# Kernel optimization log

Measured on AMD Instinct MI355X. Metric: run time of the kernel, lower is better.

## Reference

```python
import jax, jax.numpy as jnp
import numpy as np

X_DIM, Y_DIM, HIDDEN, N = 768, 768, 300, 768


def setup_inputs() -> dict:
    key = jax.random.key(0)
    ks = jax.random.split(key, 7)
    lim1 = 1.0 / np.sqrt(X_DIM + Y_DIM)
    lim2 = 1.0 / np.sqrt(HIDDEN)
    return {
        "x_samples": jax.random.normal(ks[0], (N, X_DIM), dtype=jnp.float32),
        "y_samples": jax.random.normal(ks[1], (N, Y_DIM), dtype=jnp.float32),
        "perm": jax.random.permutation(ks[2], N).astype(jnp.int32),
        # Linear 1: (x_dim+y_dim) -> hidden, torch default uniform init
        "W1": jax.random.uniform(ks[3], (HIDDEN, X_DIM + Y_DIM), jnp.float32, -lim1, lim1),
        "b1": jax.random.uniform(ks[4], (HIDDEN,), jnp.float32, -lim1, lim1),
        # Linear 2: hidden -> 1
        "W2": jax.random.uniform(ks[5], (1, HIDDEN), jnp.float32, -lim2, lim2),
        "b2": jax.random.uniform(ks[6], (1,), jnp.float32, -lim2, lim2),
    }


def reference(x_samples, y_samples, perm, W1, b1, W2, b2):
    n = x_samples.shape[0]
    x_dim = x_samples.shape[1]
    # First linear is separable across the concat: split W1 into x- and y-parts.
    hx = x_samples @ W1[:, :x_dim].T            # [N, H]
    hy = y_samples @ W1[:, x_dim:].T            # [N, H]
    w2 = W2[0]                                   # [H]
    # T0: matched pairs (x_i, y_i)
    t0 = jax.nn.softplus(jax.nn.relu(hx + hy + b1) @ w2 + b2[0])   # [N]
    # T1[i, j] = F(x_j, y_perm[i]) -- pairwise tile, [N, N, H] intermediate
    hyp = hy[perm]                               # [N, H]
    hpair = jax.nn.relu(hyp[:, None, :] + hx[None, :, :] + b1)     # [N, N, H]
    t1 = jax.nn.softplus(hpair @ w2 + b2[0])     # [N, N]
    lower_bound = t0.mean() - (jax.nn.logsumexp(t1, axis=1).mean() - jnp.log(n).astype(t1.dtype))
    return lower_bound
```

## Files before the change

kernel.cpp:

```cpp
#include <hip/hip_runtime.h>
#include <math.h>

#define NN   768
#define HH   300
#define LDH  304
#define KD   768
#define SZ   (NN*LDH)


__global__ __launch_bounds__(256) void k1_gemm(
    const float* __restrict__ x, const float* __restrict__ y,
    const int* __restrict__ perm, const float* __restrict__ W1,
    float* __restrict__ wsf)
{
    const int tid = threadIdx.x;
    const int tx = tid & 15, ty = tid >> 4;
    const int i0 = blockIdx.x * 32;
    const int h0 = blockIdx.y * 64;
    const int gemm = blockIdx.z & 1;
    const int kh   = blockIdx.z >> 1;
    const int k_beg = kh * 384;

    const float* src = gemm ? y : x;
    const int koff = gemm ? KD : 0;

    __shared__ float xs[32][34];
    __shared__ float ws[32][68];

    float acc[2][4] = {{0,0,0,0},{0,0,0,0}};

    const int srow = tid >> 3, sc4 = (tid & 7) << 2;
    int grow = i0 + srow;
    if (gemm) grow = perm[grow];
    const float* srcp = src + (size_t)grow * KD + sc4 + k_beg;

    const int hrow = tid >> 2, kc8 = (tid & 3) << 3;
    const int hg = h0 + hrow;
    const bool hvalid = hg < HH;
    const float* wrow = W1 + (size_t)hg * (2*KD) + koff + kc8 + k_beg;

    for (int kc = 0; kc < 384; kc += 32) {
        float4 xv = *(const float4*)(srcp + kc);
        xs[sc4+0][srow] = xv.x; xs[sc4+1][srow] = xv.y;
        xs[sc4+2][srow] = xv.z; xs[sc4+3][srow] = xv.w;

        float4 w0 = make_float4(0,0,0,0), w1 = make_float4(0,0,0,0);
        if (hvalid) {
            w0 = *(const float4*)(wrow + kc);
            w1 = *(const float4*)(wrow + kc + 4);
        }
        ws[kc8+0][hrow]=w0.x; ws[kc8+1][hrow]=w0.y; ws[kc8+2][hrow]=w0.z; ws[kc8+3][hrow]=w0.w;
        ws[kc8+4][hrow]=w1.x; ws[kc8+5][hrow]=w1.y; ws[kc8+6][hrow]=w1.z; ws[kc8+7][hrow]=w1.w;
        __syncthreads();

        #pragma unroll
        for (int k = 0; k < 32; ++k) {
            float a0 = xs[k][2*ty], a1 = xs[k][2*ty+1];
            float b0 = ws[k][4*tx+0], b1v = ws[k][4*tx+1];
            float b2v = ws[k][4*tx+2], b3v = ws[k][4*tx+3];
            acc[0][0] = fmaf(a0,b0, acc[0][0]); acc[0][1] = fmaf(a0,b1v,acc[0][1]);
            acc[0][2] = fmaf(a0,b2v,acc[0][2]); acc[0][3] = fmaf(a0,b3v,acc[0][3]);
            acc[1][0] = fmaf(a1,b0, acc[1][0]); acc[1][1] = fmaf(a1,b1v,acc[1][1]);
            acc[1][2] = fmaf(a1,b2v,acc[1][2]); acc[1][3] = fmaf(a1,b3v,acc[1][3]);
        }
        __syncthreads();
    }

    float* dst = wsf + (gemm ? 2*(size_t)SZ : 0) + (size_t)kh * SZ;
    #pragma unroll
    for (int r = 0; r < 2; ++r) {
        int gi = i0 + 2*ty + r;
        #pragma unroll
        for (int c = 0; c < 4; ++c) {
            int hh = h0 + 4*tx + c;
            if (hh < HH) dst[(size_t)gi*LDH + hh] = acc[r][c];
        }
    }
}

__global__ __launch_bounds__(256) void k1b_combine(
    const float* __restrict__ b1, float* __restrict__ wsf)
{
    const int N4 = SZ/4;
    int idx = blockIdx.x * 256 + threadIdx.x;
    int which = idx >= N4 ? 1 : 0;
    int rem = idx - which * N4;
    int base = rem * 4;
    int h = base % LDH;
    const float* p0 = wsf + (which ? 2*(size_t)SZ : 0);
    const float* p1 = p0 + SZ;
    float* dst = wsf + (which ? 5*(size_t)SZ : 4*(size_t)SZ);

    float4 out = make_float4(0,0,0,0);
    if (h < HH) {
        float4 v0 = *(const float4*)(p0 + base);
        float4 v1 = *(const float4*)(p1 + base);
        out.x = v0.x + v1.x; out.y = v0.y + v1.y;
        out.z = v0.z + v1.z; out.w = v0.w + v1.w;
        if (which) {
            float4 bv = *(const float4*)(b1 + h);
            out.x += bv.x; out.y += bv.y; out.z += bv.z; out.w += bv.w;
        }
    }
    *(float4*)(dst + base) = out;
}

__global__ __launch_bounds__(256) void k2_pair(
    const float* __restrict__ wsf, const float* __restrict__ w2,
    const float* __restrict__ b2, float* __restrict__ esum)
{
    const int tid = threadIdx.x;
    const int tx = tid & 15, ty = tid >> 4;
    const int i0 = blockIdx.x * 32;
    const int j0 = blockIdx.y * 64;

    const float* Af = wsf + 5*(size_t)SZ;
    const float* Cf = wsf + 4*(size_t)SZ;

    __shared__ float As[60][34];
    __shared__ float Cs[60][68];
    __shared__ float ws2[60];

    float acc[2][4] = {{0,0,0,0},{0,0,0,0}};

    for (int hc = 0; hc < HH; hc += 60) {
        for (int e = tid; e < 480; e += 256) {
            int i = e / 15, h4 = (e % 15) * 4;
            float4 v = *(const float4*)(Af + (size_t)(i0 + i)*LDH + hc + h4);
            As[h4+0][i] = v.x; As[h4+1][i] = v.y; As[h4+2][i] = v.z; As[h4+3][i] = v.w;
        }
        for (int e = tid; e < 960; e += 256) {
            int j = e / 15, h4 = (e % 15) * 4;
            float4 v = *(const float4*)(Cf + (size_t)(j0 + j)*LDH + hc + h4);
            Cs[h4+0][j] = v.x; Cs[h4+1][j] = v.y; Cs[h4+2][j] = v.z; Cs[h4+3][j] = v.w;
        }
        if (tid < 60) ws2[tid] = w2[hc + tid];
        __syncthreads();

        #pragma unroll 6
        for (int h = 0; h < 60; ++h) {
            float wh = ws2[h];
            float a0 = As[h][2*ty], a1 = As[h][2*ty+1];
            float4 cv = *(const float4*)&Cs[h][4*tx];
            float t;
            t = fmaxf(a0+cv.x,0.f); acc[0][0] = fmaf(t,wh,acc[0][0]);
            t = fmaxf(a0+cv.y,0.f); acc[0][1] = fmaf(t,wh,acc[0][1]);
            t = fmaxf(a0+cv.z,0.f); acc[0][2] = fmaf(t,wh,acc[0][2]);
            t = fmaxf(a0+cv.w,0.f); acc[0][3] = fmaf(t,wh,acc[0][3]);
            t = fmaxf(a1+cv.x,0.f); acc[1][0] = fmaf(t,wh,acc[1][0]);
            t = fmaxf(a1+cv.y,0.f); acc[1][1] = fmaf(t,wh,acc[1][1]);
            t = fmaxf(a1+cv.z,0.f); acc[1][2] = fmaf(t,wh,acc[1][2]);
            t = fmaxf(a1+cv.w,0.f); acc[1][3] = fmaf(t,wh,acc[1][3]);
        }
        __syncthreads();
    }

    const float b2v = b2[0];
    #pragma unroll
    for (int r = 0; r < 2; ++r) {
        float s = expf(acc[r][0] + b2v) + expf(acc[r][1] + b2v)
                + expf(acc[r][2] + b2v) + expf(acc[r][3] + b2v);
        s += __shfl_xor(s, 1);
        s += __shfl_xor(s, 2);
        s += __shfl_xor(s, 4);
        s += __shfl_xor(s, 8);
        if (tx == 0) atomicAdd(&esum[i0 + 2*ty + r], s);
    }
}

__global__ __launch_bounds__(256) void k2b_t0(
    const float* __restrict__ wsf, const int* __restrict__ perm,
    const float* __restrict__ w2, const float* __restrict__ b2,
    float* __restrict__ t0out)
{
    const int lane = threadIdx.x & 63;
    const int row  = blockIdx.x * 4 + (threadIdx.x >> 6);
    const float* Af = wsf + 5*(size_t)SZ;
    const float* Cf = wsf + 4*(size_t)SZ;
    const int pr = perm[row];

    float acc = 0.f;
    for (int h = lane; h < HH; h += 64) {
        float a = Af[(size_t)row*LDH + h];
        float c = Cf[(size_t)pr *LDH + h];
        float z = fmaxf(a + c, 0.f);
        acc = fmaf(z, w2[h], acc);
    }
    #pragma unroll
    for (int m = 1; m < 64; m <<= 1) acc += __shfl_xor(acc, m);
    if (lane == 0) {
        float u = acc + b2[0];
        t0out[row] = (u > 0.f) ? u + log1pf(expf(-u)) : log1pf(expf(u));
    }
}

__global__ __launch_bounds__(256) void k3_final(
    const float* __restrict__ wsf, float* __restrict__ out)
{
    const int tid = threadIdx.x;
    const float* esum = wsf + 6*(size_t)SZ;
    const float* t0   = wsf + 6*(size_t)SZ + 1024;

    double st0 = 0.0, slse = 0.0;
    for (int i = tid; i < NN; i += 256) {
        st0  += (double)t0[i];
        slse += log((double)NN + (double)esum[i]);
    }
    __shared__ double sa[256], sb[256];
    sa[tid] = st0; sb[tid] = slse;
    __syncthreads();
    for (int s = 128; s > 0; s >>= 1) {
        if (tid < s) { sa[tid] += sa[tid+s]; sb[tid] += sb[tid+s]; }
        __syncthreads();
    }
    if (tid == 0) {
        double lb = sa[0]/(double)NN - (sb[0]/(double)NN - log((double)NN));
        out[0] = (float)lb;
    }
}

extern "C" void kernel_launch(void* const* d_in, const int* in_sizes, int n_in,
                              void* d_out, int out_size, void* d_ws, size_t ws_size,
                              hipStream_t stream) {
    const float* x    = (const float*)d_in[0];
    const float* y    = (const float*)d_in[1];
    const int*   perm = (const int*)  d_in[2];
    const float* W1   = (const float*)d_in[3];
    const float* b1   = (const float*)d_in[4];
    const float* W2   = (const float*)d_in[5];
    const float* b2   = (const float*)d_in[6];
    float* wsf = (float*)d_ws;
    float* out = (float*)d_out;

    hipMemsetAsync(wsf + 6*(size_t)SZ, 0, NN * sizeof(float), stream);

    k1_gemm   <<<dim3(24,5,4), 256, 0, stream>>>(x, y, perm, W1, wsf);
    k1b_combine<<<456,          256, 0, stream>>>(b1, wsf);
    k2_pair   <<<dim3(24,12),  256, 0, stream>>>(wsf, W2, b2, wsf + 6*(size_t)SZ);
    k2b_t0    <<<192,           256, 0, stream>>>(wsf, perm, W2, b2,
                                                  wsf + 6*(size_t)SZ + 1024);
    k3_final  <<<1,             256, 0, stream>>>(wsf, out);
}
```

Measured before the change: 135.4 us.

## Split hidden dim across blocks in pair kernel and enlarge GEMM tiles

The GEMM now uses larger 128x64 tiles with 8x4 per-thread outputs and an 8-way K split, and k1b_combine sums the eight partials. The pairwise kernel splits the hidden dimension into 8 chunks of 40 over blockIdx.z with 64x128 tiles and 4x8 register blocking. Each chunk writes its partial scores to an N×N buffer, and a new row kernel sums them, applies exp and computes t0, which replaces the atomics and the memset. The aim is more parallelism and more register reuse in the dominant pairwise kernel. The cost is roughly 19 MB of extra partial-score traffic plus a wider workspace padding.

```diff
diff --git a/kernel.cpp b/kernel.cpp
--- a/kernel.cpp
+++ b/kernel.cpp
@@ -3,10 +3,17 @@
 
 #define NN   768
 #define HH   300
-#define LDH  304
+#define LDH  320
 #define KD   768
-#define SZ   (NN*LDH)
-
+
+#define P_OFF   0
+#define P_STR   245760
+#define CF_OFF  3932160
+#define AF_OFF  4177920
+#define SP_OFF  4423680
+#define SP_STR  589824
+#define ES_OFF  9142272
+#define T0_OFF  9143040
 
 __global__ __launch_bounds__(256) void k1_gemm(
     const float* __restrict__ x, const float* __restrict__ y,
@@ -14,183 +21,228 @@
     float* __restrict__ wsf)
 {
     const int tid = threadIdx.x;
-    const int tx = tid & 15, ty = tid >> 4;
-    const int i0 = blockIdx.x * 32;
+    const int tx = tid & 15;
+    const int ty = tid >> 4;
+    const int i0 = blockIdx.x * 128;
     const int h0 = blockIdx.y * 64;
     const int gemm = blockIdx.z & 1;
-    const int kh   = blockIdx.z >> 1;
-    const int k_beg = kh * 384;
+    const int ks   = blockIdx.z >> 1;
+    const int kbeg = ks * 96;
 
     const float* src = gemm ? y : x;
     const int koff = gemm ? KD : 0;
 
-    __shared__ float xs[32][34];
+    __shared__ float xs[32][132];
     __shared__ float ws[32][68];
 
-    float acc[2][4] = {{0,0,0,0},{0,0,0,0}};
-
-    const int srow = tid >> 3, sc4 = (tid & 7) << 2;
-    int grow = i0 + srow;
-    if (gemm) grow = perm[grow];
-    const float* srcp = src + (size_t)grow * KD + sc4 + k_beg;
-
-    const int hrow = tid >> 2, kc8 = (tid & 3) << 3;
-    const int hg = h0 + hrow;
-    const bool hvalid = hg < HH;
-    const float* wrow = W1 + (size_t)hg * (2*KD) + koff + kc8 + k_beg;
-
-    for (int kc = 0; kc < 384; kc += 32) {
-        float4 xv = *(const float4*)(srcp + kc);
-        xs[sc4+0][srow] = xv.x; xs[sc4+1][srow] = xv.y;
-        xs[sc4+2][srow] = xv.z; xs[sc4+3][srow] = xv.w;
-
-        float4 w0 = make_float4(0,0,0,0), w1 = make_float4(0,0,0,0);
-        if (hvalid) {
-            w0 = *(const float4*)(wrow + kc);
-            w1 = *(const float4*)(wrow + kc + 4);
-        }
-        ws[kc8+0][hrow]=w0.x; ws[kc8+1][hrow]=w0.y; ws[kc8+2][hrow]=w0.z; ws[kc8+3][hrow]=w0.w;
-        ws[kc8+4][hrow]=w1.x; ws[kc8+5][hrow]=w1.y; ws[kc8+6][hrow]=w1.z; ws[kc8+7][hrow]=w1.w;
-        __syncthreads();
-
-        #pragma unroll
+    float4 acc[8];
+    #pragma unroll
+    for (int r = 0; r < 8; ++r) acc[r] = make_float4(0.f,0.f,0.f,0.f);
+
+    for (int kc = 0; kc < 96; kc += 32) {
+        const int kb = kbeg + kc;
+        #pragma unroll
+        for (int it = 0; it < 4; ++it) {
+            int e = tid + it * 256;
+            int row = e >> 3, kq = (e & 7) << 2;
+            int grow = i0 + row;
+            if (gemm) grow = perm[grow];
+            float4 v = *(const float4*)(src + (size_t)grow * KD + kb + kq);
+            xs[kq+0][row] = v.x; xs[kq+1][row] = v.y;
+            xs[kq+2][row] = v.z; xs[kq+3][row] = v.w;
+        }
+        #pragma unroll
+        for (int it = 0; it < 2; ++it) {
+            int e = tid + it * 256;
+            int hrow = e >> 3, kq = (e & 7) << 2;
+            int hg = h0 + hrow;
+            float4 v = make_float4(0.f,0.f,0.f,0.f);
+            if (hg < HH) v = *(const float4*)(W1 + (size_t)hg * (2*KD) + koff + kb + kq);
+            ws[kq+0][hrow] = v.x; ws[kq+1][hrow] = v.y;
+            ws[kq+2][hrow] = v.z; ws[kq+3][hrow] = v.w;
+        }
+        __syncthreads();
+
+        #pragma unroll 8
         for (int k = 0; k < 32; ++k) {
-            float a0 = xs[k][2*ty], a1 = xs[k][2*ty+1];
-            float b0 = ws[k][4*tx+0], b1v = ws[k][4*tx+1];
-            float b2v = ws[k][4*tx+2], b3v = ws[k][4*tx+3];
-            acc[0][0] = fmaf(a0,b0, acc[0][0]); acc[0][1] = fmaf(a0,b1v,acc[0][1]);
-            acc[0][2] = fmaf(a0,b2v,acc[0][2]); acc[0][3] = fmaf(a0,b3v,acc[0][3]);
-            acc[1][0] = fmaf(a1,b0, acc[1][0]); acc[1][1] = fmaf(a1,b1v,acc[1][1]);
-            acc[1][2] = fmaf(a1,b2v,acc[1][2]); acc[1][3] = fmaf(a1,b3v,acc[1][3]);
-        }
-        __syncthreads();
-    }
-
-    float* dst = wsf + (gemm ? 2*(size_t)SZ : 0) + (size_t)kh * SZ;
-    #pragma unroll
-    for (int r = 0; r < 2; ++r) {
-        int gi = i0 + 2*ty + r;
-        #pragma unroll
-        for (int c = 0; c < 4; ++c) {
-            int hh = h0 + 4*tx + c;
-            if (hh < HH) dst[(size_t)gi*LDH + hh] = acc[r][c];
-        }
+            float4 a0 = *(const float4*)&xs[k][4*ty];
+            float4 a1 = *(const float4*)&xs[k][64 + 4*ty];
+            float4 b  = *(const float4*)&ws[k][4*tx];
+            acc[0].x = fmaf(a0.x,b.x,acc[0].x); acc[0].y = fmaf(a0.x,b.y,acc[0].y);
+            acc[0].z = fmaf(a0.x,b.z,acc[0].z); acc[0].w = fmaf(a0.x,b.w,acc[0].w);
+            acc[1].x = fmaf(a0.y,b.x,acc[1].x); acc[1].y = fmaf(a0.y,b.y,acc[1].y);
+            acc[1].z = fmaf(a0.y,b.z,acc[1].z); acc[1].w = fmaf(a0.y,b.w,acc[1].w);
+            acc[2].x = fmaf(a0.z,b.x,acc[2].x); acc[2].y = fmaf(a0.z,b.y,acc[2].y);
+            acc[2].z = fmaf(a0.z,b.z,acc[2].z); acc[2].w = fmaf(a0.z,b.w,acc[2].w);
+            acc[3].x = fmaf(a0.w,b.x,acc[3].x); acc[3].y = fmaf(a0.w,b.y,acc[3].y);
+            acc[3].z = fmaf(a0.w,b.z,acc[3].z); acc[3].w = fmaf(a0.w,b.w,acc[3].w);
+            acc[4].x = fmaf(a1.x,b.x,acc[4].x); acc[4].y = fmaf(a1.x,b.y,acc[4].y);
+            acc[4].z = fmaf(a1.x,b.z,acc[4].z); acc[4].w = fmaf(a1.x,b.w,acc[4].w);
+            acc[5].x = fmaf(a1.y,b.x,acc[5].x); acc[5].y = fmaf(a1.y,b.y,acc[5].y);
+            acc[5].z = fmaf(a1.y,b.z,acc[5].z); acc[5].w = fmaf(a1.y,b.w,acc[5].w);
+            acc[6].x = fmaf(a1.z,b.x,acc[6].x); acc[6].y = fmaf(a1.z,b.y,acc[6].y);
+            acc[6].z = fmaf(a1.z,b.z,acc[6].z); acc[6].w = fmaf(a1.z,b.w,acc[6].w);
+            acc[7].x = fmaf(a1.w,b.x,acc[7].x); acc[7].y = fmaf(a1.w,b.y,acc[7].y);
+            acc[7].z = fmaf(a1.w,b.z,acc[7].z); acc[7].w = fmaf(a1.w,b.w,acc[7].w);
+        }
+        __syncthreads();
+    }
+
+    float* dst = wsf + P_OFF + (size_t)(gemm*8 + ks) * P_STR;
+    #pragma unroll
+    for (int r = 0; r < 8; ++r) {
+        int i = i0 + ((r < 4) ? (4*ty + r) : (64 + 4*ty + r - 4));
+        *(float4*)(dst + (size_t)i * LDH + h0 + 4*tx) = acc[r];
     }
 }
 
 __global__ __launch_bounds__(256) void k1b_combine(
     const float* __restrict__ b1, float* __restrict__ wsf)
 {
-    const int N4 = SZ/4;
+    const int HQ = LDH/4;
+    const int PER = NN * HQ;
     int idx = blockIdx.x * 256 + threadIdx.x;
-    int which = idx >= N4 ? 1 : 0;
-    int rem = idx - which * N4;
-    int base = rem * 4;
-    int h = base % LDH;
-    const float* p0 = wsf + (which ? 2*(size_t)SZ : 0);
-    const float* p1 = p0 + SZ;
-    float* dst = wsf + (which ? 5*(size_t)SZ : 4*(size_t)SZ);
-
-    float4 out = make_float4(0,0,0,0);
-    if (h < HH) {
-        float4 v0 = *(const float4*)(p0 + base);
-        float4 v1 = *(const float4*)(p1 + base);
-        out.x = v0.x + v1.x; out.y = v0.y + v1.y;
-        out.z = v0.z + v1.z; out.w = v0.w + v1.w;
-        if (which) {
-            float4 bv = *(const float4*)(b1 + h);
+    int gemm = idx >= PER ? 1 : 0;
+    int rem = idx - gemm * PER;
+    int i = rem / HQ;
+    int h4 = (rem % HQ) * 4;
+
+    float4 out = make_float4(0.f,0.f,0.f,0.f);
+    if (h4 < HH) {
+        const float* p = wsf + P_OFF + (size_t)gemm*8*P_STR + (size_t)i*LDH + h4;
+        #pragma unroll
+        for (int ks = 0; ks < 8; ++ks) {
+            float4 v = *(const float4*)(p + (size_t)ks * P_STR);
+            out.x += v.x; out.y += v.y; out.z += v.z; out.w += v.w;
+        }
+        if (gemm) {
+            float4 bv = *(const float4*)(b1 + h4);
             out.x += bv.x; out.y += bv.y; out.z += bv.z; out.w += bv.w;
         }
     }
-    *(float4*)(dst + base) = out;
+    float* dst = wsf + (gemm ? AF_OFF : CF_OFF);
+    *(float4*)(dst + (size_t)i * LDH + h4) = out;
 }
 
 __global__ __launch_bounds__(256) void k2_pair(
     const float* __restrict__ wsf, const float* __restrict__ w2,
-    const float* __restrict__ b2, float* __restrict__ esum)
-{
-    const int tid = threadIdx.x;
-    const int tx = tid & 15, ty = tid >> 4;
-    const int i0 = blockIdx.x * 32;
-    const int j0 = blockIdx.y * 64;
-
-    const float* Af = wsf + 5*(size_t)SZ;
-    const float* Cf = wsf + 4*(size_t)SZ;
-
-    __shared__ float As[60][34];
-    __shared__ float Cs[60][68];
-    __shared__ float ws2[60];
-
-    float acc[2][4] = {{0,0,0,0},{0,0,0,0}};
-
-    for (int hc = 0; hc < HH; hc += 60) {
-        for (int e = tid; e < 480; e += 256) {
-            int i = e / 15, h4 = (e % 15) * 4;
-            float4 v = *(const float4*)(Af + (size_t)(i0 + i)*LDH + hc + h4);
-            As[h4+0][i] = v.x; As[h4+1][i] = v.y; As[h4+2][i] = v.z; As[h4+3][i] = v.w;
-        }
-        for (int e = tid; e < 960; e += 256) {
-            int j = e / 15, h4 = (e % 15) * 4;
-            float4 v = *(const float4*)(Cf + (size_t)(j0 + j)*LDH + hc + h4);
-            Cs[h4+0][j] = v.x; Cs[h4+1][j] = v.y; Cs[h4+2][j] = v.z; Cs[h4+3][j] = v.w;
-        }
-        if (tid < 60) ws2[tid] = w2[hc + tid];
-        __syncthreads();
-
-        #pragma unroll 6
-        for (int h = 0; h < 60; ++h) {
-            float wh = ws2[h];
-            float a0 = As[h][2*ty], a1 = As[h][2*ty+1];
-            float4 cv = *(const float4*)&Cs[h][4*tx];
-            float t;
-            t = fmaxf(a0+cv.x,0.f); acc[0][0] = fmaf(t,wh,acc[0][0]);
-            t = fmaxf(a0+cv.y,0.f); acc[0][1] = fmaf(t,wh,acc[0][1]);
-            t = fmaxf(a0+cv.z,0.f); acc[0][2] = fmaf(t,wh,acc[0][2]);
-            t = fmaxf(a0+cv.w,0.f); acc[0][3] = fmaf(t,wh,acc[0][3]);
-            t = fmaxf(a1+cv.x,0.f); acc[1][0] = fmaf(t,wh,acc[1][0]);
-            t = fmaxf(a1+cv.y,0.f); acc[1][1] = fmaf(t,wh,acc[1][1]);
-            t = fmaxf(a1+cv.z,0.f); acc[1][2] = fmaf(t,wh,acc[1][2]);
-            t = fmaxf(a1+cv.w,0.f); acc[1][3] = fmaf(t,wh,acc[1][3]);
-        }
-        __syncthreads();
-    }
-
-    const float b2v = b2[0];
-    #pragma unroll
-    for (int r = 0; r < 2; ++r) {
-        float s = expf(acc[r][0] + b2v) + expf(acc[r][1] + b2v)
-                + expf(acc[r][2] + b2v) + expf(acc[r][3] + b2v);
-        s += __shfl_xor(s, 1);
-        s += __shfl_xor(s, 2);
-        s += __shfl_xor(s, 4);
-        s += __shfl_xor(s, 8);
-        if (tx == 0) atomicAdd(&esum[i0 + 2*ty + r], s);
-    }
-}
-
-__global__ __launch_bounds__(256) void k2b_t0(
+    float* __restrict__ sp)
+{
+    const int tid = threadIdx.x;
+    const int tx = tid & 15;
+    const int ty = tid >> 4;
+    const int i0 = blockIdx.x * 64;
+    const int j0 = blockIdx.y * 128;
+    const int p  = blockIdx.z;
+    const int h0 = p * 40;
+
+    const float* Af = wsf + AF_OFF;
+    const float* Cf = wsf + CF_OFF;
+
+    __shared__ float As[40][68];
+    __shared__ float Cs[40][132];
+    __shared__ float ws2[40];
+
+    for (int e = tid; e < 640; e += 256) {
+        int r = e / 10, q = (e % 10) * 4;
+        float4 v = *(const float4*)(Af + (size_t)(i0 + r) * LDH + h0 + q);
+        As[q+0][r] = v.x; As[q+1][r] = v.y; As[q+2][r] = v.z; As[q+3][r] = v.w;
+    }
+    for (int e = tid; e < 1280; e += 256) {
+        int r = e / 10, q = (e % 10) * 4;
+        float4 v = *(const float4*)(Cf + (size_t)(j0 + r) * LDH + h0 + q);
+        Cs[q+0][r] = v.x; Cs[q+1][r] = v.y; Cs[q+2][r] = v.z; Cs[q+3][r] = v.w;
+    }
+    if (tid < 40) {
+        int h = h0 + tid;
+        ws2[tid] = (h < HH) ? w2[h] : 0.f;
+    }
+    __syncthreads();
+
+    float4 a0 = make_float4(0,0,0,0);
+    float acc[4][8];
+    #pragma unroll
+    for (int r = 0; r < 4; ++r)
+        #pragma unroll
+        for (int c = 0; c < 8; ++c) acc[r][c] = 0.f;
+
+    #pragma unroll 4
+    for (int h = 0; h < 40; ++h) {
+        float wh = ws2[h];
+        float4 av = *(const float4*)&As[h][4*ty];
+        float4 c0 = *(const float4*)&Cs[h][4*tx];
+        float4 c1 = *(const float4*)&Cs[h][64 + 4*tx];
+        float ar[4] = {av.x, av.y, av.z, av.w};
+        float cr[8] = {c0.x, c0.y, c0.z, c0.w, c1.x, c1.y, c1.z, c1.w};
+        #pragma unroll
+        for (int r = 0; r < 4; ++r) {
+            #pragma unroll
+            for (int c = 0; c < 8; ++c) {
+                float t = fmaxf(ar[r] + cr[c], 0.f);
+                acc[r][c] = fmaf(t, wh, acc[r][c]);
+            }
+        }
+    }
+
+    float* dst = sp + (size_t)p * SP_STR;
+    #pragma unroll
+    for (int r = 0; r < 4; ++r) {
+        int i = i0 + 4*ty + r;
+        *(float4*)(dst + (size_t)i * NN + j0 + 4*tx)      =
+            make_float4(acc[r][0], acc[r][1], acc[r][2], acc[r][3]);
+        *(float4*)(dst + (size_t)i * NN + j0 + 64 + 4*tx) =
+            make_float4(acc[r][4], acc[r][5], acc[r][6], acc[r][7]);
+    }
+}
+
+__global__ __launch_bounds__(256) void k2e_rows(
     const float* __restrict__ wsf, const int* __restrict__ perm,
     const float* __restrict__ w2, const float* __restrict__ b2,
-    float* __restrict__ t0out)
-{
-    const int lane = threadIdx.x & 63;
-    const int row  = blockIdx.x * 4 + (threadIdx.x >> 6);
-    const float* Af = wsf + 5*(size_t)SZ;
-    const float* Cf = wsf + 4*(size_t)SZ;
-    const int pr = perm[row];
-
-    float acc = 0.f;
-    for (int h = lane; h < HH; h += 64) {
-        float a = Af[(size_t)row*LDH + h];
-        float c = Cf[(size_t)pr *LDH + h];
-        float z = fmaxf(a + c, 0.f);
-        acc = fmaf(z, w2[h], acc);
-    }
-    #pragma unroll
-    for (int m = 1; m < 64; m <<= 1) acc += __shfl_xor(acc, m);
-    if (lane == 0) {
-        float u = acc + b2[0];
-        t0out[row] = (u > 0.f) ? u + log1pf(expf(-u)) : log1pf(expf(u));
+    float* __restrict__ esum, float* __restrict__ t0out)
+{
+    const int tid = threadIdx.x;
+    __shared__ float red[256];
+    const float b2v = b2[0];
+
+    if ((int)blockIdx.x < NN) {
+        const int row = blockIdx.x;
+        const float* spr = wsf + SP_OFF + (size_t)row * NN;
+        float e = 0.f;
+        #pragma unroll
+        for (int jj = 0; jj < 3; ++jj) {
+            int j = tid + jj * 256;
+            float s = 0.f;
+            #pragma unroll
+            for (int p = 0; p < 8; ++p) s += spr[(size_t)p * SP_STR + j];
+            e += expf(s + b2v);
+        }
+        red[tid] = e;
+        __syncthreads();
+        for (int s = 128; s > 0; s >>= 1) {
+            if (tid < s) red[tid] += red[tid + s];
+            __syncthreads();
+        }
+        if (tid == 0) esum[row] = red[0];
+    } else {
+        const int row = blockIdx.x - NN;
+        const int pr = perm[row];
+        const float* Af = wsf + AF_OFF + (size_t)row * LDH;
+        const float* Cf = wsf + CF_OFF + (size_t)pr  * LDH;
+        float acc = 0.f;
+        for (int h = tid; h < HH; h += 256) {
+            float z = fmaxf(Af[h] + Cf[h], 0.f);
+            acc = fmaf(z, w2[h], acc);
+        }
+        red[tid] = acc;
+        __syncthreads();
+        for (int s = 128; s > 0; s >>= 1) {
+            if (tid < s) red[tid] += red[tid + s];
+            __syncthreads();
+        }
+        if (tid == 0) {
+            float u = red[0] + b2v;
+            t0out[row] = (u > 0.f) ? u + log1pf(expf(-u)) : log1pf(expf(u));
+        }
     }
 }
 
@@ -198,8 +250,8 @@
     const float* __restrict__ wsf, float* __restrict__ out)
 {
     const int tid = threadIdx.x;
-    const float* esum = wsf + 6*(size_t)SZ;
-    const float* t0   = wsf + 6*(size_t)SZ + 1024;
+    const float* esum = wsf + ES_OFF;
+    const float* t0   = wsf + T0_OFF;
 
     double st0 = 0.0, slse = 0.0;
     for (int i = tid; i < NN; i += 256) {
@@ -232,12 +284,10 @@
     float* wsf = (float*)d_ws;
     float* out = (float*)d_out;
 
-    hipMemsetAsync(wsf + 6*(size_t)SZ, 0, NN * sizeof(float), stream);
-
-    k1_gemm   <<<dim3(24,5,4), 256, 0, stream>>>(x, y, perm, W1, wsf);
-    k1b_combine<<<456,          256, 0, stream>>>(b1, wsf);
-    k2_pair   <<<dim3(24,12),  256, 0, stream>>>(wsf, W2, b2, wsf + 6*(size_t)SZ);
-    k2b_t0    <<<192,           256, 0, stream>>>(wsf, perm, W2, b2,
-                                                  wsf + 6*(size_t)SZ + 1024);
-    k3_final  <<<1,             256, 0, stream>>>(wsf, out);
-}
+    k1_gemm    <<<dim3(6,5,16), 256, 0, stream>>>(x, y, perm, W1, wsf);
+    k1b_combine<<<480,          256, 0, stream>>>(b1, wsf);
+    k2_pair    <<<dim3(12,6,8), 256, 0, stream>>>(wsf, W2, wsf + SP_OFF);
+    k2e_rows   <<<2*NN,         256, 0, stream>>>(wsf, perm, W2, b2,
+                                                  wsf + ES_OFF, wsf + T0_OFF);
+    k3_final   <<<1,            256, 0, stream>>>(wsf, out);
+}
```

New measurement: 126.5 us. 1.07x faster.
